# Performance work log

Measured on AMD Instinct MI355X. Metric: run time of the kernel, lower is better.

The kernel has to match this reference:

```python
import jax, jax.numpy as jnp
import numpy as np

INS, OUTS = 768, 64
B, S = 8, 2048


def setup_inputs() -> dict:
    key = jax.random.key(0)
    ks = jax.random.split(key, 7)
    scale = 1.0 / np.sqrt(INS)
    inputs = jax.random.normal(ks[0], (B, S, INS), dtype=jnp.float32)
    Wq = jax.random.uniform(ks[1], (INS, OUTS), jnp.float32, -scale, scale)
    bq = jax.random.uniform(ks[2], (OUTS,), jnp.float32, -scale, scale)
    Wk = jax.random.uniform(ks[3], (INS, OUTS), jnp.float32, -scale, scale)
    bk = jax.random.uniform(ks[4], (OUTS,), jnp.float32, -scale, scale)
    Wv = jax.random.uniform(ks[5], (INS, OUTS), jnp.float32, -scale, scale)
    bv = jax.random.uniform(ks[6], (OUTS,), jnp.float32, -scale, scale)
    return {"inputs": inputs, "Wq": Wq, "bq": bq, "Wk": Wk, "bk": bk, "Wv": Wv, "bv": bv}


def reference(inputs, Wq, bq, Wk, bk, Wv, bv):
    # QKV projections: [B, S, ins] @ [ins, outs] -> [B, S, outs]
    q = jnp.einsum('bsi,io->bso', inputs, Wq) + bq
    k = jnp.einsum('bsi,io->bso', inputs, Wk) + bk
    v = jnp.einsum('bsi,io->bso', inputs, Wv) + bv
    dim_k = k.shape[-1]
    # scores: [B, S, S] (materialized, as in the original bmm-based impl)
    att = jnp.einsum('bqd,bkd->bqk', q, k) / jnp.sqrt(jnp.asarray(dim_k, q.dtype))
    att_soft = jax.nn.softmax(att, axis=-1)
    out = jnp.einsum('bqk,bkd->bqd', att_soft, v)
    return out
```

## Files before the change

### kernel.cpp

```cpp
#include <hip/hip_runtime.h>
#include <hip/hip_bf16.h>
#include <stdint.h>

#define INS 768
#define OUTS 64
#define BB 8
#define SS 2048
#define LDP 40

typedef __attribute__((ext_vector_type(8))) short short8;
typedef __attribute__((ext_vector_type(4))) float f32x4;

__device__ inline unsigned short f2bf(float f) {
  union { float f; uint32_t u; } v; v.f = f;
  uint32_t r = v.u + 0x7FFFu + ((v.u >> 16) & 1u);
  return (unsigned short)(r >> 16);
}

__device__ inline short8 cvt8hw(float4 a, float4 b) {
  union { __hip_bfloat162 h[4]; short8 s; } u;
  u.h[0] = __float22bfloat162_rn(make_float2(a.x, a.y));
  u.h[1] = __float22bfloat162_rn(make_float2(a.z, a.w));
  u.h[2] = __float22bfloat162_rn(make_float2(b.x, b.y));
  u.h[3] = __float22bfloat162_rn(make_float2(b.z, b.w));
  return u.s;
}

__device__ inline void gl_lds16(const void* g, void* l) {
  __builtin_amdgcn_global_load_lds(
      (const __attribute__((address_space(1))) uint32_t*)g,
      (__attribute__((address_space(3))) uint32_t*)l, 16, 0, 0);
}

__device__ inline void memfence_sched() { asm volatile("" ::: "memory"); }

#define PIPE_BARRIER(N)                                        \
  do {                                                         \
    asm volatile("s_waitcnt vmcnt(" #N ")" ::: "memory");      \
    __builtin_amdgcn_s_barrier();                              \
    __builtin_amdgcn_sched_barrier(0);                         \
  } while (0)

__global__ __launch_bounds__(256) void prep(
    const float* __restrict__ Wq, const float* __restrict__ Wk,
    const float* __restrict__ Wv, unsigned short* __restrict__ WT) {
  const int idx = blockIdx.x * 256 + threadIdx.x;
  const int m = idx / (INS * OUTS);
  const int r = idx - m * (INS * OUTS);
  const int k = r >> 6, n = r & 63;
  const float* W = (m == 0) ? Wq : (m == 1) ? Wk : Wv;
  const float s = (m == 0) ? 0.125f : 1.0f;
  WT[((size_t)m * OUTS + n) * INS + k] = f2bf(W[(size_t)k * OUTS + n] * s);
}

__global__ __launch_bounds__(256) void qkv(
    const float* __restrict__ X, const unsigned short* __restrict__ WT,
    const float* __restrict__ bq, const float* __restrict__ bk,
    const float* __restrict__ bv,
    unsigned short* __restrict__ Qg, unsigned short* __restrict__ Kg,
    unsigned short* __restrict__ Vtg) {
  __shared__ __align__(16) float Xs[4][1024];
  const int tid  = threadIdx.x;
  const int wave = tid >> 6, lane = tid & 63;
  const int quad = lane >> 4, l16 = lane & 15;
  const int chg  = wave;
  const int row0 = blockIdx.x * 32;

  const int sr = tid >> 3, ss = tid & 7;
  const char* gsrc =
      (const char*)(X + (size_t)(row0 + sr) * INS) + ((ss ^ (sr & 7)) << 4);
  char* ldsb = (char*)&Xs[0][0] + wave * 1024;

  const float* Bm[3]; float scl[3]; int col0[3];
  const unsigned short* Wt[3];
#pragma unroll
  for (int nt = 0; nt < 3; ++nt) {
    const int n0 = chg * 48 + nt * 16;
    const int mat = n0 >> 6;
    col0[nt] = n0 & 63;
    Wt[nt] = WT + ((size_t)mat * OUTS + col0[nt] + l16) * INS + quad * 8;
    if (mat == 0)      { Bm[nt] = bq; scl[nt] = 0.125f; }
    else if (mat == 1) { Bm[nt] = bk; scl[nt] = 1.0f; }
    else               { Bm[nt] = bv; scl[nt] = 1.0f; }
  }

  int off0[2], off1[2];
#pragma unroll
  for (int fr = 0; fr < 2; ++fr) {
    const int lr = fr * 16 + l16;
    off0[fr] = lr * 128 + ((((quad << 1)    ) ^ (lr & 7)) << 4);
    off1[fr] = lr * 128 + ((((quad << 1) | 1) ^ (lr & 7)) << 4);
  }

  f32x4 acc[2][3];
#pragma unroll
  for (int fr = 0; fr < 2; ++fr)
#pragma unroll
    for (int nt = 0; nt < 3; ++nt) acc[fr][nt] = (f32x4){0.f, 0.f, 0.f, 0.f};

  short8 wb[3][3];

  gl_lds16(gsrc, ldsb);
#pragma unroll
  for (int nt = 0; nt < 3; ++nt)
    wb[0][nt] = *reinterpret_cast<const short8*>(Wt[nt]);
  memfence_sched();
  gl_lds16(gsrc + 128, ldsb + 4096);
  gl_lds16(gsrc + 256, ldsb + 8192);
#pragma unroll
  for (int nt = 0; nt < 3; ++nt)
    wb[1][nt] = *reinterpret_cast<const short8*>(Wt[nt] + 32);

#pragma unroll
  for (int kc = 0; kc < 24; ++kc) {
    if (kc <= 21)      PIPE_BARRIER(4);
    else if (kc == 22) PIPE_BARRIER(3);
    else               PIPE_BARRIER(0);

    const char* xb = (const char*)&Xs[kc & 3][0];
    float4 f00 = *reinterpret_cast<const float4*>(xb + off0[0]);
    float4 f01 = *reinterpret_cast<const float4*>(xb + off1[0]);
    float4 f10 = *reinterpret_cast<const float4*>(xb + off0[1]);
    float4 f11 = *reinterpret_cast<const float4*>(xb + off1[1]);
    short8 a0 = cvt8hw(f00, f01);
    short8 a1 = cvt8hw(f10, f11);
#pragma unroll
    for (int nt = 0; nt < 3; ++nt) {
      acc[0][nt] = __builtin_amdgcn_mfma_f32_16x16x32_bf16(a0, wb[kc % 3][nt], acc[0][nt], 0, 0, 0);
      acc[1][nt] = __builtin_amdgcn_mfma_f32_16x16x32_bf16(a1, wb[kc % 3][nt], acc[1][nt], 0, 0, 0);
    }
    if (kc + 3 < 24)
      gl_lds16(gsrc + (size_t)(kc + 3) * 128, ldsb + (size_t)((kc + 3) & 3) * 4096);
    if (kc + 2 < 24) {
#pragma unroll
      for (int nt = 0; nt < 3; ++nt)
        wb[(kc + 2) % 3][nt] =
            *reinterpret_cast<const short8*>(Wt[nt] + (kc + 2) * 32);
    }
  }

#pragma unroll
  for (int fr = 0; fr < 2; ++fr) {
    const int gm0 = row0 + fr * 16 + quad * 4;
#pragma unroll
    for (int nt = 0; nt < 3; ++nt) {
      const int n = chg * 48 + nt * 16 + l16;
      const float bias = Bm[nt][col0[nt] + l16] * scl[nt];
      if (n < 128) {
        unsigned short* dstbase = (n < 64) ? Qg : Kg;
        const int nn = n & 63;
#pragma unroll
        for (int r = 0; r < 4; ++r)
          dstbase[(size_t)(gm0 + r) * OUTS + nn] = f2bf(acc[fr][nt][r] + bias);
      } else {
        const int d = n - 128;
        const int batch = gm0 >> 11, s0 = gm0 & 2047;
        ushort4 pk;
        pk.x = f2bf(acc[fr][nt][0] + bias);
        pk.y = f2bf(acc[fr][nt][1] + bias);
        pk.z = f2bf(acc[fr][nt][2] + bias);
        pk.w = f2bf(acc[fr][nt][3] + bias);
        *reinterpret_cast<ushort4*>(&Vtg[((size_t)batch * OUTS + d) * SS + s0]) = pk;
      }
    }
  }
}

__global__ __launch_bounds__(256) void attn(
    const unsigned short* __restrict__ Qg, const unsigned short* __restrict__ Kg,
    const unsigned short* __restrict__ Vtg,
    float* __restrict__ OP, float* __restrict__ LS) {
  __shared__ __align__(16) char KsB[4][4096];
  __shared__ __align__(16) char VsB[4][4096];
  __shared__ __align__(16) unsigned short Ps[4][2][16 * LDP];
  const int tid  = threadIdx.x;
  const int wave = tid >> 6, lane = tid & 63;
  const int quad = lane >> 4, l16 = lane & 15;
  const int bt  = blockIdx.x >> 6;
  const int rem = blockIdx.x & 63;
  const int qb  = rem >> 2, ksl = rem & 3;
  const int q0 = qb * 128 + wave * 32;
  const unsigned short* Qb = Qg + (size_t)bt * SS * OUTS;
  const unsigned short* Kb = Kg + (size_t)bt * SS * OUTS;
  const unsigned short* Vb = Vtg + (size_t)bt * OUTS * SS;
  const int jbeg = ksl * 512;

  const int krow = wave * 8 + (lane >> 3), ks8 = lane & 7;
  const int vrow = wave * 16 + (lane >> 2), vs4 = lane & 3;
  const int vsw  = (vrow & 3) ^ ((vrow >> 2) & 3);
  const char* ksrc = (const char*)(Kb + (size_t)(jbeg + krow) * OUTS) +
                     ((ks8 ^ (krow & 7)) << 4);
  const char* vsrc = (const char*)(Vb + (size_t)vrow * SS + jbeg) +
                     ((vs4 ^ vsw) << 4);

  short8 aq[2][2];
#pragma unroll
  for (int mh = 0; mh < 2; ++mh)
#pragma unroll
    for (int ks = 0; ks < 2; ++ks)
      aq[mh][ks] = *reinterpret_cast<const short8*>(
          Qb + (size_t)(q0 + mh * 16 + l16) * OUTS + ks * 32 + quad * 8);

  int koff[2][2];
#pragma unroll
  for (int nt2 = 0; nt2 < 2; ++nt2)
#pragma unroll
    for (int ks = 0; ks < 2; ++ks)
      koff[nt2][ks] = (nt2 * 16 + l16) * 128 +
                      ((((ks << 2) | quad) ^ (l16 & 7)) << 4);
  int voff[4];
#pragma unroll
  for (int nt = 0; nt < 4; ++nt) {
    const int dr = nt * 16 + l16;
    voff[nt] = dr * 64 + ((quad ^ ((dr & 3) ^ ((dr >> 2) & 3))) << 4);
  }

  f32x4 oacc[2][4];
#pragma unroll
  for (int mh = 0; mh < 2; ++mh)
#pragma unroll
    for (int nt = 0; nt < 4; ++nt) oacc[mh][nt] = (f32x4){0.f, 0.f, 0.f, 0.f};
  float lsum[2][4] = {{0.f,0.f,0.f,0.f},{0.f,0.f,0.f,0.f}};

  memfence_sched();
  gl_lds16(ksrc,                      &KsB[0][0] + wave * 1024);
  gl_lds16(vsrc,                      &VsB[0][0] + wave * 1024);
  gl_lds16(ksrc + (size_t)1 * 4096,   &KsB[1][0] + wave * 1024);
  gl_lds16(vsrc + (size_t)1 * 64,     &VsB[1][0] + wave * 1024);
  gl_lds16(ksrc + (size_t)2 * 4096,   &KsB[2][0] + wave * 1024);
  gl_lds16(vsrc + (size_t)2 * 64,     &VsB[2][0] + wave * 1024);

#pragma unroll
  for (int kc = 0; kc < 16; ++kc) {
    if (kc <= 13)      PIPE_BARRIER(4);
    else if (kc == 14) PIPE_BARRIER(2);
    else               PIPE_BARRIER(0);

    const char* kb8 = &KsB[kc & 3][0];
    const char* vb8 = &VsB[kc & 3][0];
    short8 bk[2][2], bv[4];
#pragma unroll
    for (int nt2 = 0; nt2 < 2; ++nt2)
#pragma unroll
      for (int ks = 0; ks < 2; ++ks)
        bk[nt2][ks] = *reinterpret_cast<const short8*>(kb8 + koff[nt2][ks]);
#pragma unroll
    for (int nt = 0; nt < 4; ++nt)
      bv[nt] = *reinterpret_cast<const short8*>(vb8 + voff[nt]);

#pragma unroll
    for (int mh = 0; mh < 2; ++mh) {
      f32x4 sc[2];
      sc[0] = (f32x4){0.f,0.f,0.f,0.f}; sc[1] = (f32x4){0.f,0.f,0.f,0.f};
#pragma unroll
      for (int ks = 0; ks < 2; ++ks)
#pragma unroll
        for (int nt2 = 0; nt2 < 2; ++nt2)
          sc[nt2] = __builtin_amdgcn_mfma_f32_16x16x32_bf16(aq[mh][ks], bk[nt2][ks], sc[nt2], 0, 0, 0);

      unsigned short* Pw = Ps[wave][mh];
#pragma unroll
      for (int nt2 = 0; nt2 < 2; ++nt2)
#pragma unroll
        for (int r = 0; r < 4; ++r) {
          float p = __expf(sc[nt2][r]);
          lsum[mh][r] += p;
          Pw[(quad * 4 + r) * LDP + nt2 * 16 + l16] = f2bf(p);
        }
      short8 ap = *reinterpret_cast<const short8*>(&Pw[l16 * LDP + quad * 8]);
#pragma unroll
      for (int nt = 0; nt < 4; ++nt)
        oacc[mh][nt] = __builtin_amdgcn_mfma_f32_16x16x32_bf16(ap, bv[nt], oacc[mh][nt], 0, 0, 0);
    }

    if (kc + 3 < 16) {
      gl_lds16(ksrc + (size_t)(kc + 3) * 4096, &KsB[(kc + 3) & 3][0] + wave * 1024);
      gl_lds16(vsrc + (size_t)(kc + 3) * 64,   &VsB[(kc + 3) & 3][0] + wave * 1024);
    }
  }

#pragma unroll
  for (int st = 1; st < 16; st <<= 1)
#pragma unroll
    for (int mh = 0; mh < 2; ++mh)
#pragma unroll
      for (int r = 0; r < 4; ++r) lsum[mh][r] += __shfl_xor(lsum[mh][r], st, 64);

  float* OPb = OP + ((size_t)ksl * BB + bt) * SS * OUTS;
#pragma unroll
  for (int mh = 0; mh < 2; ++mh)
#pragma unroll
    for (int nt = 0; nt < 4; ++nt)
#pragma unroll
      for (int r = 0; r < 4; ++r) {
        int q = q0 + mh * 16 + quad * 4 + r;
        OPb[(size_t)q * OUTS + nt * 16 + l16] = oacc[mh][nt][r];
      }
  if (l16 == 0) {
#pragma unroll
    for (int mh = 0; mh < 2; ++mh)
#pragma unroll
      for (int r = 0; r < 4; ++r)
        LS[(size_t)ksl * BB * SS + bt * SS + q0 + mh * 16 + quad * 4 + r] = lsum[mh][r];
  }
}

__global__ __launch_bounds__(256) void combine(
    const float* __restrict__ OP, const float* __restrict__ LS,
    float* __restrict__ out) {
  const size_t i4 = (size_t)blockIdx.x * 256 + threadIdx.x;
  const size_t row = (i4 * 4) >> 6;
  float4 o = make_float4(0.f, 0.f, 0.f, 0.f);
  float l = 0.f;
#pragma unroll
  for (int ks = 0; ks < 4; ++ks) {
    float4 t = reinterpret_cast<const float4*>(OP + (size_t)ks * BB * SS * OUTS)[i4];
    o.x += t.x; o.y += t.y; o.z += t.z; o.w += t.w;
    l += LS[(size_t)ks * BB * SS + row];
  }
  const float inv = 1.0f / l;
  reinterpret_cast<float4*>(out)[i4] = make_float4(o.x * inv, o.y * inv, o.z * inv, o.w * inv);
}

extern "C" void kernel_launch(void* const* d_in, const int* in_sizes, int n_in,
                              void* d_out, int out_size, void* d_ws, size_t ws_size,
                              hipStream_t stream) {
  const float* X  = (const float*)d_in[0];
  const float* Wq = (const float*)d_in[1];
  const float* bq = (const float*)d_in[2];
  const float* Wk = (const float*)d_in[3];
  const float* bk = (const float*)d_in[4];
  const float* Wv = (const float*)d_in[5];
  const float* bv = (const float*)d_in[6];
  float* out = (float*)d_out;

  char* ws = (char*)d_ws;
  unsigned short* Qg  = (unsigned short*)(ws);
  unsigned short* Kg  = (unsigned short*)(ws + (size_t)2 * 1024 * 1024);
  unsigned short* Vtg = (unsigned short*)(ws + (size_t)4 * 1024 * 1024);
  unsigned short* WT  = (unsigned short*)(ws + (size_t)6 * 1024 * 1024);
  float*          OP  = (float*)(ws + (size_t)7 * 1024 * 1024);
  float*          LS  = (float*)(ws + (size_t)23 * 1024 * 1024);

  prep<<<576, 256, 0, stream>>>(Wq, Wk, Wv, WT);
  qkv<<<512, 256, 0, stream>>>(X, WT, bq, bk, bv, Qg, Kg, Vtg);
  attn<<<512, 256, 0, stream>>>(Qg, Kg, Vtg, OP, LS);
  combine<<<1024, 256, 0, stream>>>(OP, LS, out);
}
```

Measured before the change: 138.4 us.

## Split attention keys into eight slices and wrap QKV projection in repeat loop

The attention kernel now splits each batch's key range into eight 256-key slices instead of four 512-key slices. That doubles the grid to 1024 blocks and adds an occupancy hint to the launch bounds, aiming for better GPU fill. The K/V LDS staging drops from four buffers to three, with prefetch depth 2, to cut shared memory per block. The combine kernel now sums eight partials, and the workspace offset for the row sums moves to fit the larger partial buffer. The QKV projection body is also wrapped in a non-unrolled loop that recomputes and rewrites identical results three times. That adds redundant global reads of X and redundant stores, which looks like a timing experiment.

```diff
diff --git a/kernel.cpp b/kernel.cpp
--- a/kernel.cpp
+++ b/kernel.cpp
@@ -92,98 +92,102 @@
     off1[fr] = lr * 128 + ((((quad << 1) | 1) ^ (lr & 7)) << 4);
   }
 
-  f32x4 acc[2][3];
-#pragma unroll
-  for (int fr = 0; fr < 2; ++fr)
-#pragma unroll
-    for (int nt = 0; nt < 3; ++nt) acc[fr][nt] = (f32x4){0.f, 0.f, 0.f, 0.f};
-
-  short8 wb[3][3];
-
-  gl_lds16(gsrc, ldsb);
-#pragma unroll
-  for (int nt = 0; nt < 3; ++nt)
-    wb[0][nt] = *reinterpret_cast<const short8*>(Wt[nt]);
-  memfence_sched();
-  gl_lds16(gsrc + 128, ldsb + 4096);
-  gl_lds16(gsrc + 256, ldsb + 8192);
-#pragma unroll
-  for (int nt = 0; nt < 3; ++nt)
-    wb[1][nt] = *reinterpret_cast<const short8*>(Wt[nt] + 32);
-
-#pragma unroll
-  for (int kc = 0; kc < 24; ++kc) {
-    if (kc <= 21)      PIPE_BARRIER(4);
-    else if (kc == 22) PIPE_BARRIER(3);
-    else               PIPE_BARRIER(0);
-
-    const char* xb = (const char*)&Xs[kc & 3][0];
-    float4 f00 = *reinterpret_cast<const float4*>(xb + off0[0]);
-    float4 f01 = *reinterpret_cast<const float4*>(xb + off1[0]);
-    float4 f10 = *reinterpret_cast<const float4*>(xb + off0[1]);
-    float4 f11 = *reinterpret_cast<const float4*>(xb + off1[1]);
-    short8 a0 = cvt8hw(f00, f01);
-    short8 a1 = cvt8hw(f10, f11);
-#pragma unroll
-    for (int nt = 0; nt < 3; ++nt) {
-      acc[0][nt] = __builtin_amdgcn_mfma_f32_16x16x32_bf16(a0, wb[kc % 3][nt], acc[0][nt], 0, 0, 0);
-      acc[1][nt] = __builtin_amdgcn_mfma_f32_16x16x32_bf16(a1, wb[kc % 3][nt], acc[1][nt], 0, 0, 0);
-    }
-    if (kc + 3 < 24)
-      gl_lds16(gsrc + (size_t)(kc + 3) * 128, ldsb + (size_t)((kc + 3) & 3) * 4096);
-    if (kc + 2 < 24) {
-#pragma unroll
-      for (int nt = 0; nt < 3; ++nt)
-        wb[(kc + 2) % 3][nt] =
-            *reinterpret_cast<const short8*>(Wt[nt] + (kc + 2) * 32);
-    }
-  }
-
-#pragma unroll
-  for (int fr = 0; fr < 2; ++fr) {
-    const int gm0 = row0 + fr * 16 + quad * 4;
-#pragma unroll
-    for (int nt = 0; nt < 3; ++nt) {
-      const int n = chg * 48 + nt * 16 + l16;
-      const float bias = Bm[nt][col0[nt] + l16] * scl[nt];
-      if (n < 128) {
-        unsigned short* dstbase = (n < 64) ? Qg : Kg;
-        const int nn = n & 63;
-#pragma unroll
-        for (int r = 0; r < 4; ++r)
-          dstbase[(size_t)(gm0 + r) * OUTS + nn] = f2bf(acc[fr][nt][r] + bias);
-      } else {
-        const int d = n - 128;
-        const int batch = gm0 >> 11, s0 = gm0 & 2047;
-        ushort4 pk;
-        pk.x = f2bf(acc[fr][nt][0] + bias);
-        pk.y = f2bf(acc[fr][nt][1] + bias);
-        pk.z = f2bf(acc[fr][nt][2] + bias);
-        pk.w = f2bf(acc[fr][nt][3] + bias);
-        *reinterpret_cast<ushort4*>(&Vtg[((size_t)batch * OUTS + d) * SS + s0]) = pk;
+#pragma unroll 1
+  for (int rep = 0; rep < 3; ++rep) {
+    f32x4 acc[2][3];
+#pragma unroll
+    for (int fr = 0; fr < 2; ++fr)
+#pragma unroll
+      for (int nt = 0; nt < 3; ++nt) acc[fr][nt] = (f32x4){0.f, 0.f, 0.f, 0.f};
+
+    short8 wb[3][3];
+
+    memfence_sched();
+    gl_lds16(gsrc, ldsb);
+#pragma unroll
+    for (int nt = 0; nt < 3; ++nt)
+      wb[0][nt] = *reinterpret_cast<const short8*>(Wt[nt]);
+    memfence_sched();
+    gl_lds16(gsrc + 128, ldsb + 4096);
+    gl_lds16(gsrc + 256, ldsb + 8192);
+#pragma unroll
+    for (int nt = 0; nt < 3; ++nt)
+      wb[1][nt] = *reinterpret_cast<const short8*>(Wt[nt] + 32);
+
+#pragma unroll
+    for (int kc = 0; kc < 24; ++kc) {
+      if (kc <= 21)      PIPE_BARRIER(4);
+      else if (kc == 22) PIPE_BARRIER(3);
+      else               PIPE_BARRIER(0);
+
+      const char* xb = (const char*)&Xs[0][0] + (kc & 3) * 4096;
+      float4 f00 = *reinterpret_cast<const float4*>(xb + off0[0]);
+      float4 f01 = *reinterpret_cast<const float4*>(xb + off1[0]);
+      float4 f10 = *reinterpret_cast<const float4*>(xb + off0[1]);
+      float4 f11 = *reinterpret_cast<const float4*>(xb + off1[1]);
+      short8 a0 = cvt8hw(f00, f01);
+      short8 a1 = cvt8hw(f10, f11);
+#pragma unroll
+      for (int nt = 0; nt < 3; ++nt) {
+        acc[0][nt] = __builtin_amdgcn_mfma_f32_16x16x32_bf16(a0, wb[kc % 3][nt], acc[0][nt], 0, 0, 0);
+        acc[1][nt] = __builtin_amdgcn_mfma_f32_16x16x32_bf16(a1, wb[kc % 3][nt], acc[1][nt], 0, 0, 0);
+      }
+      if (kc + 3 < 24)
+        gl_lds16(gsrc + (size_t)(kc + 3) * 128, ldsb + (size_t)((kc + 3) & 3) * 4096);
+      if (kc + 2 < 24) {
+#pragma unroll
+        for (int nt = 0; nt < 3; ++nt)
+          wb[(kc + 2) % 3][nt] =
+              *reinterpret_cast<const short8*>(Wt[nt] + (kc + 2) * 32);
       }
     }
-  }
-}
-
-__global__ __launch_bounds__(256) void attn(
+
+#pragma unroll
+    for (int fr = 0; fr < 2; ++fr) {
+      const int gm0 = row0 + fr * 16 + quad * 4;
+#pragma unroll
+      for (int nt = 0; nt < 3; ++nt) {
+        const int n = chg * 48 + nt * 16 + l16;
+        const float bias = Bm[nt][col0[nt] + l16] * scl[nt];
+        if (n < 128) {
+          unsigned short* dstbase = (n < 64) ? Qg : Kg;
+          const int nn = n & 63;
+#pragma unroll
+          for (int r = 0; r < 4; ++r)
+            dstbase[(size_t)(gm0 + r) * OUTS + nn] = f2bf(acc[fr][nt][r] + bias);
+        } else {
+          const int d = n - 128;
+          const int batch = gm0 >> 11, s0 = gm0 & 2047;
+          ushort4 pk;
+          pk.x = f2bf(acc[fr][nt][0] + bias);
+          pk.y = f2bf(acc[fr][nt][1] + bias);
+          pk.z = f2bf(acc[fr][nt][2] + bias);
+          pk.w = f2bf(acc[fr][nt][3] + bias);
+          *reinterpret_cast<ushort4*>(&Vtg[((size_t)batch * OUTS + d) * SS + s0]) = pk;
+        }
+      }
+    }
+  }
+}
+
+__global__ __launch_bounds__(256, 4) void attn(
     const unsigned short* __restrict__ Qg, const unsigned short* __restrict__ Kg,
     const unsigned short* __restrict__ Vtg,
     float* __restrict__ OP, float* __restrict__ LS) {
-  __shared__ __align__(16) char KsB[4][4096];
-  __shared__ __align__(16) char VsB[4][4096];
+  __shared__ __align__(16) char KsB[3][4096];
+  __shared__ __align__(16) char VsB[3][4096];
   __shared__ __align__(16) unsigned short Ps[4][2][16 * LDP];
   const int tid  = threadIdx.x;
   const int wave = tid >> 6, lane = tid & 63;
   const int quad = lane >> 4, l16 = lane & 15;
-  const int bt  = blockIdx.x >> 6;
-  const int rem = blockIdx.x & 63;
-  const int qb  = rem >> 2, ksl = rem & 3;
+  const int bt  = blockIdx.x >> 7;
+  const int rem = blockIdx.x & 127;
+  const int qb  = rem >> 3, ksl = rem & 7;
   const int q0 = qb * 128 + wave * 32;
   const unsigned short* Qb = Qg + (size_t)bt * SS * OUTS;
   const unsigned short* Kb = Kg + (size_t)bt * SS * OUTS;
   const unsigned short* Vb = Vtg + (size_t)bt * OUTS * SS;
-  const int jbeg = ksl * 512;
+  const int jbeg = ksl * 256;
 
   const int krow = wave * 8 + (lane >> 3), ks8 = lane & 7;
   const int vrow = wave * 16 + (lane >> 2), vs4 = lane & 3;
@@ -193,6 +197,12 @@
   const char* vsrc = (const char*)(Vb + (size_t)vrow * SS + jbeg) +
                      ((vs4 ^ vsw) << 4);
 
+#define STAGE(kc)                                                            \
+  do {                                                                       \
+    gl_lds16(ksrc + (size_t)(kc) * 4096, &KsB[(kc) % 3][0] + wave * 1024);   \
+    gl_lds16(vsrc + (size_t)(kc) * 64,   &VsB[(kc) % 3][0] + wave * 1024);   \
+  } while (0)
+
   short8 aq[2][2];
 #pragma unroll
   for (int mh = 0; mh < 2; ++mh)
@@ -223,21 +233,16 @@
   float lsum[2][4] = {{0.f,0.f,0.f,0.f},{0.f,0.f,0.f,0.f}};
 
   memfence_sched();
-  gl_lds16(ksrc,                      &KsB[0][0] + wave * 1024);
-  gl_lds16(vsrc,                      &VsB[0][0] + wave * 1024);
-  gl_lds16(ksrc + (size_t)1 * 4096,   &KsB[1][0] + wave * 1024);
-  gl_lds16(vsrc + (size_t)1 * 64,     &VsB[1][0] + wave * 1024);
-  gl_lds16(ksrc + (size_t)2 * 4096,   &KsB[2][0] + wave * 1024);
-  gl_lds16(vsrc + (size_t)2 * 64,     &VsB[2][0] + wave * 1024);
-
-#pragma unroll
-  for (int kc = 0; kc < 16; ++kc) {
-    if (kc <= 13)      PIPE_BARRIER(4);
-    else if (kc == 14) PIPE_BARRIER(2);
-    else               PIPE_BARRIER(0);
-
-    const char* kb8 = &KsB[kc & 3][0];
-    const char* vb8 = &VsB[kc & 3][0];
+  STAGE(0);
+  STAGE(1);
+
+#pragma unroll
+  for (int kc = 0; kc < 8; ++kc) {
+    if (kc <= 6) PIPE_BARRIER(2);
+    else         PIPE_BARRIER(0);
+
+    const char* kb8 = &KsB[kc % 3][0];
+    const char* vb8 = &VsB[kc % 3][0];
     short8 bk[2][2], bv[4];
 #pragma unroll
     for (int nt2 = 0; nt2 < 2; ++nt2)
@@ -258,7 +263,7 @@
         for (int nt2 = 0; nt2 < 2; ++nt2)
           sc[nt2] = __builtin_amdgcn_mfma_f32_16x16x32_bf16(aq[mh][ks], bk[nt2][ks], sc[nt2], 0, 0, 0);
 
-      unsigned short* Pw = Ps[wave][mh];
+      unsigned short* Pw = &Ps[wave][mh][0];
 #pragma unroll
       for (int nt2 = 0; nt2 < 2; ++nt2)
 #pragma unroll
@@ -273,11 +278,9 @@
         oacc[mh][nt] = __builtin_amdgcn_mfma_f32_16x16x32_bf16(ap, bv[nt], oacc[mh][nt], 0, 0, 0);
     }
 
-    if (kc + 3 < 16) {
-      gl_lds16(ksrc + (size_t)(kc + 3) * 4096, &KsB[(kc + 3) & 3][0] + wave * 1024);
-      gl_lds16(vsrc + (size_t)(kc + 3) * 64,   &VsB[(kc + 3) & 3][0] + wave * 1024);
-    }
-  }
+    if (kc + 2 < 8) STAGE(kc + 2);
+  }
+#undef STAGE
 
 #pragma unroll
   for (int st = 1; st < 16; st <<= 1)
@@ -313,7 +316,7 @@
   float4 o = make_float4(0.f, 0.f, 0.f, 0.f);
   float l = 0.f;
 #pragma unroll
-  for (int ks = 0; ks < 4; ++ks) {
+  for (int ks = 0; ks < 8; ++ks) {
     float4 t = reinterpret_cast<const float4*>(OP + (size_t)ks * BB * SS * OUTS)[i4];
     o.x += t.x; o.y += t.y; o.z += t.z; o.w += t.w;
     l += LS[(size_t)ks * BB * SS + row];
@@ -340,10 +343,10 @@
   unsigned short* Vtg = (unsigned short*)(ws + (size_t)4 * 1024 * 1024);
   unsigned short* WT  = (unsigned short*)(ws + (size_t)6 * 1024 * 1024);
   float*          OP  = (float*)(ws + (size_t)7 * 1024 * 1024);
-  float*          LS  = (float*)(ws + (size_t)23 * 1024 * 1024);
+  float*          LS  = (float*)(ws + (size_t)40 * 1024 * 1024);
 
   prep<<<576, 256, 0, stream>>>(Wq, Wk, Wv, WT);
   qkv<<<512, 256, 0, stream>>>(X, WT, bq, bk, bv, Qg, Kg, Vtg);
-  attn<<<512, 256, 0, stream>>>(Qg, Kg, Vtg, OP, LS);
+  attn<<<1024, 256, 0, stream>>>(Qg, Kg, Vtg, OP, LS);
   combine<<<1024, 256, 0, stream>>>(OP, LS, out);
 }
```

Result: slower. 221.9 us (+60.4%).
